# Optimization experiments

Measured on AMD Instinct MI355X. Metric: run time of the kernel, lower is better.

The kernel has to match this reference:

```python
import jax, jax.numpy as jnp
import numpy as np

N = 100000
E = 3200000

def gcn_conv(x, W, b, src, dst, num_nodes):
    # PyG GCNConv: x' = D^-1/2 (A+I) D^-1/2 (x W) + b
    h = x @ W  # [N, out]
    # self loops appended
    src_sl = jnp.concatenate([src, jnp.arange(num_nodes)])
    dst_sl = jnp.concatenate([dst, jnp.arange(num_nodes)])
    deg = jnp.zeros((num_nodes,), h.dtype).at[dst_sl].add(1.0)
    dinv = jnp.where(deg > 0, 1.0 / jnp.sqrt(deg), 0.0)
    norm = dinv[src_sl] * dinv[dst_sl]  # [E+N]
    msgs = h[src_sl] * norm[:, None]
    out = jnp.zeros_like(h).at[dst_sl].add(msgs)
    return out + b

def setup_inputs() -> dict:
    key = jax.random.key(0)
    k1, k2, k3, k4, k5 = jax.random.split(key, 5)
    z = jax.random.normal(k1, (N, 16), dtype=jnp.float32)
    edge_index = jax.random.randint(k2, (2, E), 0, N, dtype=jnp.int64)
    W1 = jax.random.normal(k3, (16, 256), dtype=jnp.float32) * (1.0 / np.sqrt(16))
    b1 = jnp.zeros((256,), jnp.float32)
    W2 = jax.random.normal(k4, (256, 256), dtype=jnp.float32) * (1.0 / np.sqrt(256))
    b2 = jnp.zeros((256,), jnp.float32)
    return {"z": z, "edge_index": edge_index, "W1": W1, "b1": b1, "W2": W2, "b2": b2}

def reference(z, edge_index, W1, b1, W2, b2):
    src, dst = edge_index[0], edge_index[1]
    h = gcn_conv(z, W1, b1, src, dst, N)
    h = gcn_conv(h, W2, b2, src, dst, N)
    value = jnp.sum(h[src] * h[dst], axis=1)  # [E]
    return jax.nn.sigmoid(value)
```

## Files before the change

### kernel.cpp

```cpp
#include <hip/hip_runtime.h>
#include <hip/hip_fp16.h>
#include <math.h>

#define N_NODES 100000
#define N_EDGES 3200000
#define GRID_G 6250
#define NSB 782
#define SB_NODES 128
#define SBCAP 5120
#define E_BLK 12800
#define PART_BLOCKS 250
#define PART_THREADS 1024
#define GRID_DEC 12500

#define OFF_DINV 0
#define OFF_C    100016
#define OFF_ZS16 200032
#define OFF_T16  1000048
#define OFF_U    1800064
#define OFF_YT   3400080
#define OFF_ST   4200080
#define OFF_PR   6604720
#define OFF_PB   6604736
#define OFF_ABG  6604752
#define OFF_L    6604768
#define FLOAT_TOTAL 6605024
#define IOFF_GCUR 0
#define IOFF_BEG  1024
#define IOFF_CNT  101024
#define IOFF_BUF  201024
#define IOFF_CSR  4204864

__device__ inline float4 h4_to_f4(uint2 v) {
    __half2 a = *reinterpret_cast<__half2*>(&v.x);
    __half2 b = *reinterpret_cast<__half2*>(&v.y);
    float2 fa = __half22float2(a), fb = __half22float2(b);
    return make_float4(fa.x, fa.y, fb.x, fb.y);
}
__device__ inline uint2 f4_to_h4(float4 f) {
    uint2 r;
    __half2 a = __floats2half2_rn(f.x, f.y);
    __half2 b = __floats2half2_rn(f.z, f.w);
    r.x = *reinterpret_cast<unsigned*>(&a);
    r.y = *reinterpret_cast<unsigned*>(&b);
    return r;
}
__device__ inline float4 pack_h8(float4 a, float4 b) {
    float4 r;
    __half2* p = reinterpret_cast<__half2*>(&r);
    p[0] = __floats2half2_rn(a.x, a.y);
    p[1] = __floats2half2_rn(a.z, a.w);
    p[2] = __floats2half2_rn(b.x, b.y);
    p[3] = __floats2half2_rn(b.z, b.w);
    return r;
}
__device__ inline unsigned h2bits(float a, float b) {
    __half2 h = __floats2half2_rn(a, b);
    return *reinterpret_cast<unsigned*>(&h);
}
__device__ inline float2 bits2f2(unsigned v) {
    __half2 h = *reinterpret_cast<__half2*>(&v);
    return __half22float2(h);
}
__device__ inline float hdot8f(float4 a, float4 b) {
    const __half2* pa = reinterpret_cast<const __half2*>(&a);
    const __half2* pb = reinterpret_cast<const __half2*>(&b);
    float s = 0.0f;
    #pragma unroll
    for (int i = 0; i < 4; i++) {
        float2 fa = __half22float2(pa[i]);
        float2 fb = __half22float2(pb[i]);
        s += fa.x * fb.x + fa.y * fb.y;
    }
    return s;
}
__device__ inline void acc4(float4& acc, uint2 g) {
    float4 f = h4_to_f4(g);
    acc.x += f.x; acc.y += f.y; acc.z += f.z; acc.w += f.w;
}

struct ConstsSh {
    float sW1t[16 * 256];
    float sM[16 * 257];
    float sb1[256];
    float sb2[256];
    float sR[256];
    float sG[256];
    float sLf[256];
};
struct PartSh {
    int hist[4][NSB];
    int cur[NSB];
};

__global__ void __launch_bounds__(PART_THREADS)
k_part(const int* __restrict__ src, const int* __restrict__ dst,
       int* __restrict__ gcur, int* __restrict__ buf,
       const float* __restrict__ W1, const float* __restrict__ b1,
       const float* __restrict__ W2, const float* __restrict__ b2,
       float* __restrict__ ws) {
    __shared__ union { ConstsSh c; PartSh p; } sh;
    int t = threadIdx.x;

    if (blockIdx.x == PART_BLOCKS) {
        bool act = t < 256;
        if (act) {
            #pragma unroll
            for (int r = 0; r < 16; r++)
                sh.c.sW1t[t * 16 + r] = W1[r * 256 + t];
            sh.c.sb1[t] = b1[t];
            sh.c.sb2[t] = b2[t];
        }
        __syncthreads();
        if (act) {
            float acc[16];
            #pragma unroll
            for (int i = 0; i < 16; i++) acc[i] = 0.0f;
            float raccv = 0.0f;
            for (int kk = 0; kk < 256; kk += 8) {
                float w2v[8];
                #pragma unroll
                for (int u = 0; u < 8; u++)
                    w2v[u] = W2[(kk + u) * 256 + t];
                #pragma unroll
                for (int u = 0; u < 8; u++) {
                    #pragma unroll
                    for (int i = 0; i < 16; i++)
                        acc[i] += sh.c.sW1t[(kk + u) * 16 + i] * w2v[u];
                    raccv += sh.c.sb1[kk + u] * w2v[u];
                }
            }
            #pragma unroll
            for (int i = 0; i < 16; i++) sh.c.sM[i * 257 + t] = acc[i];
            sh.c.sR[t] = raccv;
        }
        __syncthreads();
        if (act) {
            int i = t >> 4, j = t & 15;
            float gg = 0.0f;
            for (int tt = 0; tt < 256; tt++)
                gg += sh.c.sM[i * 257 + tt] * sh.c.sM[j * 257 + tt];
            sh.c.sG[t] = gg;
        }
        if (t < 16) {
            float a = 0.0f, b = 0.0f;
            for (int tt = 0; tt < 256; tt++) {
                a += sh.c.sM[t * 257 + tt] * sh.c.sR[tt];
                b += sh.c.sM[t * 257 + tt] * sh.c.sb2[tt];
            }
            ws[OFF_PR + t] = a;
            ws[OFF_PB + t] = b;
        }
        if (t == 0) {
            float al = 0.0f, be = 0.0f, ga = 0.0f;
            for (int tt = 0; tt < 256; tt++) {
                al += sh.c.sR[tt] * sh.c.sR[tt];
                be += sh.c.sR[tt] * sh.c.sb2[tt];
                ga += sh.c.sb2[tt] * sh.c.sb2[tt];
            }
            float disc = sqrtf(al * al + 4.0f);
            float lp = 0.5f * (al + disc);
            float lm = 0.5f * (al - disc);
            float k1 = sqrtf(lp / (lp * lp + 1.0f));
            float k2 = sqrtf(-lm / (lm * lm + 1.0f));
            ws[OFF_ABG + 0] = be;
            ws[OFF_ABG + 1] = 0.5f * ga;
            ws[OFF_ABG + 2] = lp;
            ws[OFF_ABG + 3] = lm;
            ws[OFF_ABG + 4] = k1;
            ws[OFF_ABG + 5] = k2;
        }
        __syncthreads();
        if (act) sh.c.sLf[t] = 0.0f;
        __syncthreads();
        for (int j = 0; j < 16; j++) {
            if (t == j) {
                float s = sh.c.sG[j * 16 + j];
                for (int k = 0; k < j; k++)
                    s -= sh.c.sLf[j * 16 + k] * sh.c.sLf[j * 16 + k];
                sh.c.sLf[j * 16 + j] = sqrtf(fmaxf(s, 1e-20f));
            }
            __syncthreads();
            if (t > j && t < 16) {
                float s = sh.c.sG[t * 16 + j];
                for (int k = 0; k < j; k++)
                    s -= sh.c.sLf[t * 16 + k] * sh.c.sLf[j * 16 + k];
                sh.c.sLf[t * 16 + j] = s / sh.c.sLf[j * 16 + j];
            }
            __syncthreads();
        }
        if (act) ws[OFF_L + t] = sh.c.sLf[t];
        return;
    }

    int cp = t >> 8;
    int base = blockIdx.x * E_BLK;
    for (int i = t; i < 4 * NSB; i += PART_THREADS) ((int*)sh.p.hist)[i] = 0;
    __syncthreads();
    for (int i = t; i < E_BLK; i += PART_THREADS) {
        int e = base + i;
        if (e < N_EDGES)
            atomicAdd(&sh.p.hist[cp][__builtin_nontemporal_load(dst + e) >> 7], 1);
    }
    __syncthreads();
    for (int i = t; i < NSB; i += PART_THREADS) {
        int h = sh.p.hist[0][i] + sh.p.hist[1][i] + sh.p.hist[2][i] + sh.p.hist[3][i];
        sh.p.cur[i] = (h > 0) ? atomicAdd(&gcur[i], h) : 0;
    }
    __syncthreads();
    for (int i = t; i < E_BLK; i += PART_THREADS) {
        int e = base + i;
        if (e >= N_EDGES) continue;
        int d = __builtin_nontemporal_load(dst + e);
        int s = __builtin_nontemporal_load(src + e);
        int sb = d >> 7;
        int pos = atomicAdd(&sh.p.cur[sb], 1);
        if (pos < SBCAP) buf[sb * SBCAP + pos] = s | ((d & 127) << 17);
    }
}

__global__ void k_sort(const float* __restrict__ z, const int* __restrict__ gcur,
                       const int* __restrict__ buf, int* __restrict__ csr,
                       int* __restrict__ begA, int* __restrict__ cntA,
                       float* __restrict__ ws) {
    __shared__ int pay[SBCAP];
    __shared__ int h[SB_NODES + 1];
    __shared__ int lcur[SB_NODES];
    __shared__ float sdv[SB_NODES];
    int sb = blockIdx.x, t = threadIdx.x;
    int n = gcur[sb];
    if (n > SBCAP) n = SBCAP;
    for (int i = t; i < n; i += 256) pay[i] = buf[sb * SBCAP + i];
    if (t <= SB_NODES) h[t] = 0;
    __syncthreads();
    for (int i = t; i < n; i += 256) atomicAdd(&h[(pay[i] >> 17) + 1], 1);
    __syncthreads();
    int mydeg = 0;
    if (t < SB_NODES) { mydeg = h[t + 1]; h[t + 1] = (mydeg + 3) & ~3; }
    __syncthreads();
    for (int off = 1; off <= SB_NODES; off <<= 1) {
        int v = 0;
        if (t <= SB_NODES && t >= off) v = h[t - off];
        __syncthreads();
        if (t <= SB_NODES) h[t] += v;
        __syncthreads();
    }
    int n0 = sb * SB_NODES;
    if (t < SB_NODES) {
        lcur[t] = h[t];
        float dv = rsqrtf((float)(mydeg + 1));
        sdv[t] = dv;
        if (n0 + t < N_NODES) {
            cntA[n0 + t] = mydeg;
            begA[n0 + t] = sb * SBCAP + h[t];
            ws[OFF_DINV + n0 + t] = dv;
        }
    }
    __syncthreads();
    {
        int nl = t >> 1, half = t & 1;
        int node = n0 + nl;
        if (node < N_NODES) {
            const float4* zr = (const float4*)(z + (size_t)node * 16) + 2 * half;
            float dv = sdv[nl];
            float4 a = zr[0], b = zr[1];
            a = make_float4(a.x * dv, a.y * dv, a.z * dv, a.w * dv);
            b = make_float4(b.x * dv, b.y * dv, b.z * dv, b.w * dv);
            ((float4*)((__half*)(ws + OFF_ZS16) + (size_t)node * 16))[half] = pack_h8(a, b);
        }
    }
    for (int i = t; i < n; i += 256) {
        int p = pay[i];
        int dl = p >> 17;
        int pos = atomicAdd(&lcur[dl], 1);
        if (pos < SBCAP) csr[sb * SBCAP + pos] = p & 0x1FFFF;
    }
}

__global__ void k_gather1(const int* __restrict__ cntA, const int* __restrict__ begA,
                          const int* __restrict__ csr, float* __restrict__ ws) {
    int lane = threadIdx.x & 15;
    int g = threadIdx.x >> 4;
    int q = lane & 3;
    int sub = lane >> 2;
    int d = blockIdx.x * 16 + g;
    if (d >= N_NODES) return;
    const float* dinv = ws + OFF_DINV;
    const __half* zs = (const __half*)(ws + OFF_ZS16);
    float dd = dinv[d];
    float dv2 = dd * dd;
    int deg = cntA[d];
    int beg = begA[d];
    float4 acc = make_float4(0.f, 0.f, 0.f, 0.f);
    float csum = 0.0f;
    int j = 0;
    for (; j + 32 <= deg; j += 32) {
        int4 ia = *(const int4*)(csr + beg + j + sub * 4);
        int4 ib = *(const int4*)(csr + beg + j + 16 + sub * 4);
        uint2 g0 = ((const uint2*)(zs + (size_t)ia.x * 16))[q];
        uint2 g1 = ((const uint2*)(zs + (size_t)ia.y * 16))[q];
        uint2 g2 = ((const uint2*)(zs + (size_t)ia.z * 16))[q];
        uint2 g3 = ((const uint2*)(zs + (size_t)ia.w * 16))[q];
        uint2 g4 = ((const uint2*)(zs + (size_t)ib.x * 16))[q];
        uint2 g5 = ((const uint2*)(zs + (size_t)ib.y * 16))[q];
        uint2 g6 = ((const uint2*)(zs + (size_t)ib.z * 16))[q];
        uint2 g7 = ((const uint2*)(zs + (size_t)ib.w * 16))[q];
        float dva = 0.0f, dvb = 0.0f;
        if (q == 0) {
            dva = (dinv[ia.x] + dinv[ia.y]) + (dinv[ia.z] + dinv[ia.w]);
            dvb = (dinv[ib.x] + dinv[ib.y]) + (dinv[ib.z] + dinv[ib.w]);
        }
        __builtin_amdgcn_sched_barrier(0);
        acc4(acc, g0); acc4(acc, g1); acc4(acc, g2); acc4(acc, g3);
        acc4(acc, g4); acc4(acc, g5); acc4(acc, g6); acc4(acc, g7);
        csum += dva + dvb;
    }
    for (; j + 16 <= deg; j += 16) {
        int4 idx = *(const int4*)(csr + beg + j + sub * 4);
        uint2 g0 = ((const uint2*)(zs + (size_t)idx.x * 16))[q];
        uint2 g1 = ((const uint2*)(zs + (size_t)idx.y * 16))[q];
        uint2 g2 = ((const uint2*)(zs + (size_t)idx.z * 16))[q];
        uint2 g3 = ((const uint2*)(zs + (size_t)idx.w * 16))[q];
        acc4(acc, g0); acc4(acc, g1); acc4(acc, g2); acc4(acc, g3);
        if (q == 0) csum += (dinv[idx.x] + dinv[idx.y]) + (dinv[idx.z] + dinv[idx.w]);
    }
    for (int t = j + sub; t < deg; t += 4) {
        int s0 = csr[beg + t];
        acc4(acc, ((const uint2*)(zs + (size_t)s0 * 16))[q]);
        if (q == 0) csum += dinv[s0];
    }
    #pragma unroll
    for (int off = 4; off <= 8; off <<= 1) {
        acc.x += __shfl_xor(acc.x, off, 64);
        acc.y += __shfl_xor(acc.y, off, 64);
        acc.z += __shfl_xor(acc.z, off, 64);
        acc.w += __shfl_xor(acc.w, off, 64);
        csum  += __shfl_xor(csum,  off, 64);
    }
    if (sub == 0) {
        float4 zrow = h4_to_f4(((const uint2*)(zs + (size_t)d * 16))[q]);
        float4 o = make_float4(dv2 * (acc.x + zrow.x), dv2 * (acc.y + zrow.y),
                               dv2 * (acc.z + zrow.z), dv2 * (acc.w + zrow.w));
        ((uint2*)((__half*)(ws + OFF_T16) + (size_t)d * 16))[q] = f4_to_h4(o);
        if (q == 0) (ws + OFF_C)[d] = dd * csum + dv2;
    }
}

__global__ void k_gather2(const int* __restrict__ cntA, const int* __restrict__ begA,
                          const int* __restrict__ csr, float* __restrict__ ws) {
    __shared__ float sL[256];
    __shared__ float spr[16];
    __shared__ float spb[16];
    __shared__ float sprm[8];
    int tid = threadIdx.x;
    sL[tid] = ws[OFF_L + tid];
    if (tid < 16) { spr[tid] = ws[OFF_PR + tid]; spb[tid] = ws[OFF_PB + tid]; }
    if (tid < 8) sprm[tid] = ws[OFF_ABG + tid];
    __syncthreads();

    int lane = tid & 15;
    int g = tid >> 4;
    int q = lane & 3;
    int sub = lane >> 2;
    int d = blockIdx.x * 16 + g;
    const float* dinv = ws + OFF_DINV;
    const __half* t16 = (const __half*)(ws + OFF_T16);
    float dd = dinv[d];
    int deg = cntA[d];
    int beg = begA[d];
    float4 acc = make_float4(0.f, 0.f, 0.f, 0.f);
    int j = 0;
    for (; j + 32 <= deg; j += 32) {
        int4 ia = *(const int4*)(csr + beg + j + sub * 4);
        int4 ib = *(const int4*)(csr + beg + j + 16 + sub * 4);
        uint2 g0 = ((const uint2*)(t16 + (size_t)ia.x * 16))[q];
        uint2 g1 = ((const uint2*)(t16 + (size_t)ia.y * 16))[q];
        uint2 g2 = ((const uint2*)(t16 + (size_t)ia.z * 16))[q];
        uint2 g3 = ((const uint2*)(t16 + (size_t)ia.w * 16))[q];
        uint2 g4 = ((const uint2*)(t16 + (size_t)ib.x * 16))[q];
        uint2 g5 = ((const uint2*)(t16 + (size_t)ib.y * 16))[q];
        uint2 g6 = ((const uint2*)(t16 + (size_t)ib.z * 16))[q];
        uint2 g7 = ((const uint2*)(t16 + (size_t)ib.w * 16))[q];
        __builtin_amdgcn_sched_barrier(0);
        acc4(acc, g0); acc4(acc, g1); acc4(acc, g2); acc4(acc, g3);
        acc4(acc, g4); acc4(acc, g5); acc4(acc, g6); acc4(acc, g7);
    }
    for (; j + 16 <= deg; j += 16) {
        int4 idx = *(const int4*)(csr + beg + j + sub * 4);
        uint2 g0 = ((const uint2*)(t16 + (size_t)idx.x * 16))[q];
        uint2 g1 = ((const uint2*)(t16 + (size_t)idx.y * 16))[q];
        uint2 g2 = ((const uint2*)(t16 + (size_t)idx.z * 16))[q];
        uint2 g3 = ((const uint2*)(t16 + (size_t)idx.w * 16))[q];
        acc4(acc, g0); acc4(acc, g1); acc4(acc, g2); acc4(acc, g3);
    }
    for (int t = j + sub; t < deg; t += 4) {
        int s0 = csr[beg + t];
        acc4(acc, ((const uint2*)(t16 + (size_t)s0 * 16))[q]);
    }
    #pragma unroll
    for (int off = 4; off <= 8; off <<= 1) {
        acc.x += __shfl_xor(acc.x, off, 64);
        acc.y += __shfl_xor(acc.y, off, 64);
        acc.z += __shfl_xor(acc.z, off, 64);
        acc.w += __shfl_xor(acc.w, off, 64);
    }
    if (sub == 0) {
        float4 trow = h4_to_f4(((const uint2*)(t16 + (size_t)d * 16))[q]);
        float ux = dd * (acc.x + trow.x);
        float uy = dd * (acc.y + trow.y);
        float uz = dd * (acc.z + trow.z);
        float uw = dd * (acc.w + trow.w);
        int r0 = 4 * q;
        float pA = ux * spr[r0] + uy * spr[r0 + 1] + uz * spr[r0 + 2] + uw * spr[r0 + 3];
        float pB = ux * spb[r0] + uy * spb[r0 + 1] + uz * spb[r0 + 2] + uw * spb[r0 + 3];
        float py[16];
        #pragma unroll
        for (int jj = 0; jj < 16; jj++) {
            py[jj] = ux * sL[(r0 + 0) * 16 + jj] + uy * sL[(r0 + 1) * 16 + jj]
                   + uz * sL[(r0 + 2) * 16 + jj] + uw * sL[(r0 + 3) * 16 + jj];
        }
        #pragma unroll
        for (int jj = 0; jj < 16; jj++) {
            py[jj] += __shfl_xor(py[jj], 1, 64);
            py[jj] += __shfl_xor(py[jj], 2, 64);
        }
        pA += __shfl_xor(pA, 1, 64); pA += __shfl_xor(pA, 2, 64);
        pB += __shfl_xor(pB, 1, 64); pB += __shfl_xor(pB, 2, 64);
        uint2 yw = make_uint2(h2bits(py[r0], py[r0 + 1]), h2bits(py[r0 + 2], py[r0 + 3]));
        ((uint2*)(ws + OFF_YT))[(size_t)d * 4 + q] = yw;
        if (q == 0) {
            float beta = sprm[0], gh = sprm[1], lp = sprm[2], lm = sprm[3];
            float k1 = sprm[4], k2 = sprm[5];
            float ci = (ws + OFF_C)[d];
            float Ap = pA + beta;
            float Bp = pB + gh;
            float r1 = k1 * (lp * ci + Ap);
            float r2 = k2 * (lm * ci + Ap);
            const float inv_s2 = 0.70710678118654752f;
            float r3 = (Bp + 1.0f) * inv_s2;
            float r4 = (Bp - 1.0f) * inv_s2;
            ((uint2*)(ws + OFF_ST))[d] = make_uint2(h2bits(r1, r2), h2bits(r3, r4));
        }
    }
}

__global__ void k_decode(const int* __restrict__ src, const int* __restrict__ dst,
                         const float* __restrict__ ws, float* __restrict__ out) {
    int e = blockIdx.x * 256 + threadIdx.x;
    const float4* yt = (const float4*)(ws + OFF_YT);
    const uint2*  st = (const uint2*)(ws + OFF_ST);
    int s = __builtin_nontemporal_load(src + e);
    int d = __builtin_nontemporal_load(dst + e);
    float4 sy0 = yt[2 * (size_t)s];
    float4 sy1 = yt[2 * (size_t)s + 1];
    float4 dy0 = yt[2 * (size_t)d];
    float4 dy1 = yt[2 * (size_t)d + 1];
    uint2  ssc = st[s];
    uint2  dsc = st[d];
    __builtin_amdgcn_sched_barrier(0);
    float v = hdot8f(sy0, dy0) + hdot8f(sy1, dy1);
    float2 ra = bits2f2(ssc.x), rb = bits2f2(dsc.x);
    float2 rc = bits2f2(ssc.y), rd = bits2f2(dsc.y);
    v += ra.x * rb.x - ra.y * rb.y + rc.x * rd.x - rc.y * rd.y;
    __builtin_nontemporal_store(1.0f / (1.0f + expf(-v)), out + e);
}

extern "C" void kernel_launch(void* const* d_in, const int* in_sizes, int n_in,
                              void* d_out, int out_size, void* d_ws, size_t ws_size,
                              hipStream_t stream) {
    const float* z  = (const float*)d_in[0];
    const int*   ei = (const int*)d_in[1];
    const float* W1 = (const float*)d_in[2];
    const float* b1 = (const float*)d_in[3];
    const float* W2 = (const float*)d_in[4];
    const float* b2 = (const float*)d_in[5];
    float* out = (float*)d_out;
    float* ws  = (float*)d_ws;
    int*   wi  = (int*)(ws + FLOAT_TOTAL);

    const int* src = ei;
    const int* dst = ei + N_EDGES;

    int* gcur = wi + IOFF_GCUR;
    int* begA = wi + IOFF_BEG;
    int* cntA = wi + IOFF_CNT;
    int* buf  = wi + IOFF_BUF;
    int* csr  = wi + IOFF_CSR;

    hipMemsetAsync(gcur, 0, 1024 * sizeof(int), stream);
    k_part    <<<PART_BLOCKS + 1, PART_THREADS, 0, stream>>>(src, dst, gcur, buf,
                                                             W1, b1, W2, b2, ws);
    k_sort    <<<NSB, 256, 0, stream>>>(z, gcur, buf, csr, begA, cntA, ws);
    k_gather1 <<<GRID_G, 256, 0, stream>>>(cntA, begA, csr, ws);
    k_gather2 <<<GRID_G, 256, 0, stream>>>(cntA, begA, csr, ws);
    k_decode  <<<GRID_DEC, 256, 0, stream>>>(src, dst, ws, out);
}
```

Measured before the change: 297.2 us.

## Gather full 16-wide fp16 rows per lane instead of quarter-row slices

```diff
diff --git a/kernel.cpp b/kernel.cpp
--- a/kernel.cpp
+++ b/kernel.cpp
@@ -74,9 +74,19 @@
     }
     return s;
 }
-__device__ inline void acc4(float4& acc, uint2 g) {
-    float4 f = h4_to_f4(g);
-    acc.x += f.x; acc.y += f.y; acc.z += f.z; acc.w += f.w;
+__device__ inline void acc8(float4& lo, float4& hi, uint4 v) {
+    float2 p0 = __half22float2(*reinterpret_cast<__half2*>(&v.x));
+    float2 p1 = __half22float2(*reinterpret_cast<__half2*>(&v.y));
+    float2 p2 = __half22float2(*reinterpret_cast<__half2*>(&v.z));
+    float2 p3 = __half22float2(*reinterpret_cast<__half2*>(&v.w));
+    lo.x += p0.x; lo.y += p0.y; lo.z += p1.x; lo.w += p1.y;
+    hi.x += p2.x; hi.y += p2.y; hi.z += p3.x; hi.w += p3.y;
+}
+__device__ inline void bfly4(float4& v, int m) {
+    v.x += __shfl_xor(v.x, m, 64);
+    v.y += __shfl_xor(v.y, m, 64);
+    v.z += __shfl_xor(v.z, m, 64);
+    v.w += __shfl_xor(v.w, m, 64);
 }
 
 struct ConstsSh {
@@ -279,71 +289,57 @@
 
 __global__ void k_gather1(const int* __restrict__ cntA, const int* __restrict__ begA,
                           const int* __restrict__ csr, float* __restrict__ ws) {
-    int lane = threadIdx.x & 15;
-    int g = threadIdx.x >> 4;
-    int q = lane & 3;
-    int sub = lane >> 2;
+    int tid = threadIdx.x;
+    int lane = tid & 15;
+    int g = tid >> 4;
     int d = blockIdx.x * 16 + g;
-    if (d >= N_NODES) return;
     const float* dinv = ws + OFF_DINV;
     const __half* zs = (const __half*)(ws + OFF_ZS16);
     float dd = dinv[d];
     float dv2 = dd * dd;
     int deg = cntA[d];
     int beg = begA[d];
-    float4 acc = make_float4(0.f, 0.f, 0.f, 0.f);
+    float4 f0 = make_float4(0.f,0.f,0.f,0.f), f1 = f0, f2 = f0, f3 = f0;
     float csum = 0.0f;
-    int j = 0;
-    for (; j + 32 <= deg; j += 32) {
-        int4 ia = *(const int4*)(csr + beg + j + sub * 4);
-        int4 ib = *(const int4*)(csr + beg + j + 16 + sub * 4);
-        uint2 g0 = ((const uint2*)(zs + (size_t)ia.x * 16))[q];
-        uint2 g1 = ((const uint2*)(zs + (size_t)ia.y * 16))[q];
-        uint2 g2 = ((const uint2*)(zs + (size_t)ia.z * 16))[q];
-        uint2 g3 = ((const uint2*)(zs + (size_t)ia.w * 16))[q];
-        uint2 g4 = ((const uint2*)(zs + (size_t)ib.x * 16))[q];
-        uint2 g5 = ((const uint2*)(zs + (size_t)ib.y * 16))[q];
-        uint2 g6 = ((const uint2*)(zs + (size_t)ib.z * 16))[q];
-        uint2 g7 = ((const uint2*)(zs + (size_t)ib.w * 16))[q];
-        float dva = 0.0f, dvb = 0.0f;
-        if (q == 0) {
-            dva = (dinv[ia.x] + dinv[ia.y]) + (dinv[ia.z] + dinv[ia.w]);
-            dvb = (dinv[ib.x] + dinv[ib.y]) + (dinv[ib.z] + dinv[ib.w]);
-        }
+    int j = lane;
+    for (; j + 16 < deg; j += 32) {
+        int s0 = csr[beg + j];
+        int s1 = csr[beg + j + 16];
+        uint4 a0 = *(const uint4*)(zs + (size_t)s0 * 16);
+        uint4 a1 = *(const uint4*)(zs + (size_t)s0 * 16 + 8);
+        uint4 b0 = *(const uint4*)(zs + (size_t)s1 * 16);
+        uint4 b1 = *(const uint4*)(zs + (size_t)s1 * 16 + 8);
+        float dv = dinv[s0] + dinv[s1];
         __builtin_amdgcn_sched_barrier(0);
-        acc4(acc, g0); acc4(acc, g1); acc4(acc, g2); acc4(acc, g3);
-        acc4(acc, g4); acc4(acc, g5); acc4(acc, g6); acc4(acc, g7);
-        csum += dva + dvb;
-    }
-    for (; j + 16 <= deg; j += 16) {
-        int4 idx = *(const int4*)(csr + beg + j + sub * 4);
-        uint2 g0 = ((const uint2*)(zs + (size_t)idx.x * 16))[q];
-        uint2 g1 = ((const uint2*)(zs + (size_t)idx.y * 16))[q];
-        uint2 g2 = ((const uint2*)(zs + (size_t)idx.z * 16))[q];
-        uint2 g3 = ((const uint2*)(zs + (size_t)idx.w * 16))[q];
-        acc4(acc, g0); acc4(acc, g1); acc4(acc, g2); acc4(acc, g3);
-        if (q == 0) csum += (dinv[idx.x] + dinv[idx.y]) + (dinv[idx.z] + dinv[idx.w]);
-    }
-    for (int t = j + sub; t < deg; t += 4) {
-        int s0 = csr[beg + t];
-        acc4(acc, ((const uint2*)(zs + (size_t)s0 * 16))[q]);
-        if (q == 0) csum += dinv[s0];
+        acc8(f0, f1, a0); acc8(f2, f3, a1);
+        acc8(f0, f1, b0); acc8(f2, f3, b1);
+        csum += dv;
+    }
+    if (j < deg) {
+        int s0 = csr[beg + j];
+        uint4 a0 = *(const uint4*)(zs + (size_t)s0 * 16);
+        uint4 a1 = *(const uint4*)(zs + (size_t)s0 * 16 + 8);
+        float dv = dinv[s0];
+        __builtin_amdgcn_sched_barrier(0);
+        acc8(f0, f1, a0); acc8(f2, f3, a1);
+        csum += dv;
     }
     #pragma unroll
-    for (int off = 4; off <= 8; off <<= 1) {
-        acc.x += __shfl_xor(acc.x, off, 64);
-        acc.y += __shfl_xor(acc.y, off, 64);
-        acc.z += __shfl_xor(acc.z, off, 64);
-        acc.w += __shfl_xor(acc.w, off, 64);
-        csum  += __shfl_xor(csum,  off, 64);
-    }
-    if (sub == 0) {
-        float4 zrow = h4_to_f4(((const uint2*)(zs + (size_t)d * 16))[q]);
-        float4 o = make_float4(dv2 * (acc.x + zrow.x), dv2 * (acc.y + zrow.y),
-                               dv2 * (acc.z + zrow.z), dv2 * (acc.w + zrow.w));
-        ((uint2*)((__half*)(ws + OFF_T16) + (size_t)d * 16))[q] = f4_to_h4(o);
-        if (q == 0) (ws + OFF_C)[d] = dd * csum + dv2;
-    }
+    for (int m = 1; m <= 8; m <<= 1) {
+        bfly4(f0, m); bfly4(f1, m); bfly4(f2, m); bfly4(f3, m);
+        csum += __shfl_xor(csum, m, 64);
+    }
+    if (lane < 4) {
+        float4 zq = h4_to_f4(((const uint2*)(zs + (size_t)d * 16))[lane]);
+        float4 fq = f0;
+        if (lane == 1) fq = f1;
+        if (lane == 2) fq = f2;
+        if (lane == 3) fq = f3;
+        float4 o = make_float4(dv2 * (fq.x + zq.x), dv2 * (fq.y + zq.y),
+                               dv2 * (fq.z + zq.z), dv2 * (fq.w + zq.w));
+        ((uint2*)((__half*)(ws + OFF_T16) + (size_t)d * 16))[lane] = f4_to_h4(o);
+    }
+    if (lane == 0) (ws + OFF_C)[d] = dd * csum + dv2;
 }
 
 __global__ void k_gather2(const int* __restrict__ cntA, const int* __restrict__ begA,
@@ -360,87 +356,77 @@
 
     int lane = tid & 15;
     int g = tid >> 4;
-    int q = lane & 3;
-    int sub = lane >> 2;
     int d = blockIdx.x * 16 + g;
     const float* dinv = ws + OFF_DINV;
     const __half* t16 = (const __half*)(ws + OFF_T16);
     float dd = dinv[d];
     int deg = cntA[d];
     int beg = begA[d];
-    float4 acc = make_float4(0.f, 0.f, 0.f, 0.f);
-    int j = 0;
-    for (; j + 32 <= deg; j += 32) {
-        int4 ia = *(const int4*)(csr + beg + j + sub * 4);
-        int4 ib = *(const int4*)(csr + beg + j + 16 + sub * 4);
-        uint2 g0 = ((const uint2*)(t16 + (size_t)ia.x * 16))[q];
-        uint2 g1 = ((const uint2*)(t16 + (size_t)ia.y * 16))[q];
-        uint2 g2 = ((const uint2*)(t16 + (size_t)ia.z * 16))[q];
-        uint2 g3 = ((const uint2*)(t16 + (size_t)ia.w * 16))[q];
-        uint2 g4 = ((const uint2*)(t16 + (size_t)ib.x * 16))[q];
-        uint2 g5 = ((const uint2*)(t16 + (size_t)ib.y * 16))[q];
-        uint2 g6 = ((const uint2*)(t16 + (size_t)ib.z * 16))[q];
-        uint2 g7 = ((const uint2*)(t16 + (size_t)ib.w * 16))[q];
+    float4 f0 = make_float4(0.f,0.f,0.f,0.f), f1 = f0, f2 = f0, f3 = f0;
+    int j = lane;
+    for (; j + 16 < deg; j += 32) {
+        int s0 = csr[beg + j];
+        int s1 = csr[beg + j + 16];
+        uint4 a0 = *(const uint4*)(t16 + (size_t)s0 * 16);
+        uint4 a1 = *(const uint4*)(t16 + (size_t)s0 * 16 + 8);
+        uint4 b0 = *(const uint4*)(t16 + (size_t)s1 * 16);
+        uint4 b1 = *(const uint4*)(t16 + (size_t)s1 * 16 + 8);
         __builtin_amdgcn_sched_barrier(0);
-        acc4(acc, g0); acc4(acc, g1); acc4(acc, g2); acc4(acc, g3);
-        acc4(acc, g4); acc4(acc, g5); acc4(acc, g6); acc4(acc, g7);
-    }
-    for (; j + 16 <= deg; j += 16) {
-        int4 idx = *(const int4*)(csr + beg + j + sub * 4);
-        uint2 g0 = ((const uint2*)(t16 + (size_t)idx.x * 16))[q];
-        uint2 g1 = ((const uint2*)(t16 + (size_t)idx.y * 16))[q];
-        uint2 g2 = ((const uint2*)(t16 + (size_t)idx.z * 16))[q];
-        uint2 g3 = ((const uint2*)(t16 + (size_t)idx.w * 16))[q];
-        acc4(acc, g0); acc4(acc, g1); acc4(acc, g2); acc4(acc, g3);
-    }
-    for (int t = j + sub; t < deg; t += 4) {
-        int s0 = csr[beg + t];
-        acc4(acc, ((const uint2*)(t16 + (size_t)s0 * 16))[q]);
+        acc8(f0, f1, a0); acc8(f2, f3, a1);
+        acc8(f0, f1, b0); acc8(f2, f3, b1);
+    }
+    if (j < deg) {
+        int s0 = csr[beg + j];
+        uint4 a0 = *(const uint4*)(t16 + (size_t)s0 * 16);
+        uint4 a1 = *(const uint4*)(t16 + (size_t)s0 * 16 + 8);
+        __builtin_amdgcn_sched_barrier(0);
+        acc8(f0, f1, a0); acc8(f2, f3, a1);
     }
     #pragma unroll
-    for (int off = 4; off <= 8; off <<= 1) {
-        acc.x += __shfl_xor(acc.x, off, 64);
-        acc.y += __shfl_xor(acc.y, off, 64);
-        acc.z += __shfl_xor(acc.z, off, 64);
-        acc.w += __shfl_xor(acc.w, off, 64);
-    }
-    if (sub == 0) {
-        float4 trow = h4_to_f4(((const uint2*)(t16 + (size_t)d * 16))[q]);
-        float ux = dd * (acc.x + trow.x);
-        float uy = dd * (acc.y + trow.y);
-        float uz = dd * (acc.z + trow.z);
-        float uw = dd * (acc.w + trow.w);
-        int r0 = 4 * q;
-        float pA = ux * spr[r0] + uy * spr[r0 + 1] + uz * spr[r0 + 2] + uw * spr[r0 + 3];
-        float pB = ux * spb[r0] + uy * spb[r0 + 1] + uz * spb[r0 + 2] + uw * spb[r0 + 3];
-        float py[16];
-        #pragma unroll
-        for (int jj = 0; jj < 16; jj++) {
-            py[jj] = ux * sL[(r0 + 0) * 16 + jj] + uy * sL[(r0 + 1) * 16 + jj]
-                   + uz * sL[(r0 + 2) * 16 + jj] + uw * sL[(r0 + 3) * 16 + jj];
-        }
-        #pragma unroll
-        for (int jj = 0; jj < 16; jj++) {
-            py[jj] += __shfl_xor(py[jj], 1, 64);
-            py[jj] += __shfl_xor(py[jj], 2, 64);
-        }
-        pA += __shfl_xor(pA, 1, 64); pA += __shfl_xor(pA, 2, 64);
-        pB += __shfl_xor(pB, 1, 64); pB += __shfl_xor(pB, 2, 64);
-        uint2 yw = make_uint2(h2bits(py[r0], py[r0 + 1]), h2bits(py[r0 + 2], py[r0 + 3]));
-        ((uint2*)(ws + OFF_YT))[(size_t)d * 4 + q] = yw;
-        if (q == 0) {
-            float beta = sprm[0], gh = sprm[1], lp = sprm[2], lm = sprm[3];
-            float k1 = sprm[4], k2 = sprm[5];
-            float ci = (ws + OFF_C)[d];
-            float Ap = pA + beta;
-            float Bp = pB + gh;
-            float r1 = k1 * (lp * ci + Ap);
-            float r2 = k2 * (lm * ci + Ap);
-            const float inv_s2 = 0.70710678118654752f;
-            float r3 = (Bp + 1.0f) * inv_s2;
-            float r4 = (Bp - 1.0f) * inv_s2;
-            ((uint2*)(ws + OFF_ST))[d] = make_uint2(h2bits(r1, r2), h2bits(r3, r4));
-        }
+    for (int m = 1; m <= 8; m <<= 1) {
+        bfly4(f0, m); bfly4(f1, m); bfly4(f2, m); bfly4(f3, m);
+    }
+    uint4 t0 = *(const uint4*)(t16 + (size_t)d * 16);
+    uint4 t1 = *(const uint4*)(t16 + (size_t)d * 16 + 8);
+    float4 z0 = make_float4(0.f,0.f,0.f,0.f), z1 = z0, z2 = z0, z3 = z0;
+    acc8(z0, z1, t0); acc8(z2, z3, t1);
+    float4 u0 = make_float4(dd*(f0.x+z0.x), dd*(f0.y+z0.y), dd*(f0.z+z0.z), dd*(f0.w+z0.w));
+    float4 u1 = make_float4(dd*(f1.x+z1.x), dd*(f1.y+z1.y), dd*(f1.z+z1.z), dd*(f1.w+z1.w));
+    float4 u2 = make_float4(dd*(f2.x+z2.x), dd*(f2.y+z2.y), dd*(f2.z+z2.z), dd*(f2.w+z2.w));
+    float4 u3 = make_float4(dd*(f3.x+z3.x), dd*(f3.y+z3.y), dd*(f3.z+z3.z), dd*(f3.w+z3.w));
+    float yl = u0.x * sL[0*16+lane]  + u0.y * sL[1*16+lane]
+             + u0.z * sL[2*16+lane]  + u0.w * sL[3*16+lane]
+             + u1.x * sL[4*16+lane]  + u1.y * sL[5*16+lane]
+             + u1.z * sL[6*16+lane]  + u1.w * sL[7*16+lane]
+             + u2.x * sL[8*16+lane]  + u2.y * sL[9*16+lane]
+             + u2.z * sL[10*16+lane] + u2.w * sL[11*16+lane]
+             + u3.x * sL[12*16+lane] + u3.y * sL[13*16+lane]
+             + u3.z * sL[14*16+lane] + u3.w * sL[15*16+lane];
+    float yn = __shfl_xor(yl, 1, 64);
+    unsigned w = h2bits(yl, yn);
+    unsigned w2 = __shfl_xor(w, 2, 64);
+    if ((lane & 3) == 0)
+        ((uint2*)(ws + OFF_YT))[(size_t)d * 4 + (lane >> 2)] = make_uint2(w, w2);
+    if (lane == 0) {
+        float pA = u0.x*spr[0]  + u0.y*spr[1]  + u0.z*spr[2]  + u0.w*spr[3]
+                 + u1.x*spr[4]  + u1.y*spr[5]  + u1.z*spr[6]  + u1.w*spr[7]
+                 + u2.x*spr[8]  + u2.y*spr[9]  + u2.z*spr[10] + u2.w*spr[11]
+                 + u3.x*spr[12] + u3.y*spr[13] + u3.z*spr[14] + u3.w*spr[15];
+        float pB = u0.x*spb[0]  + u0.y*spb[1]  + u0.z*spb[2]  + u0.w*spb[3]
+                 + u1.x*spb[4]  + u1.y*spb[5]  + u1.z*spb[6]  + u1.w*spb[7]
+                 + u2.x*spb[8]  + u2.y*spb[9]  + u2.z*spb[10] + u2.w*spb[11]
+                 + u3.x*spb[12] + u3.y*spb[13] + u3.z*spb[14] + u3.w*spb[15];
+        float beta = sprm[0], gh = sprm[1], lp = sprm[2], lm = sprm[3];
+        float k1 = sprm[4], k2 = sprm[5];
+        float ci = (ws + OFF_C)[d];
+        float Ap = pA + beta;
+        float Bp = pB + gh;
+        float r1 = k1 * (lp * ci + Ap);
+        float r2 = k2 * (lm * ci + Ap);
+        const float inv_s2 = 0.70710678118654752f;
+        float r3 = (Bp + 1.0f) * inv_s2;
+        float r4 = (Bp - 1.0f) * inv_s2;
+        ((uint2*)(ws + OFF_ST))[d] = make_uint2(h2bits(r1, r2), h2bits(r3, r4));
     }
 }
 
```

Result: slower. 322.8 us (+8.6%).
